# Kernel optimization log

Hardware: AMD Instinct MI355X
Metric: run time of the kernel (lower is better)

## Reference

```python
import jax, jax.numpy as jnp
import numpy as np

D_MODEL = 768
D_STATE = 16
EXPAND = 2
D_INNER = D_MODEL * EXPAND
K_CONV = 4
RMS_EPS = 1.1920928955078125e-07  # torch.finfo(float32).eps (nn.RMSNorm default eps=None)


def setup_inputs() -> dict:
    key = jax.random.key(0)
    ks = jax.random.split(key, 8)
    x = jax.random.normal(ks[0], (2, 2048, D_MODEL), dtype=jnp.float32)
    # parameters (torch Linear stores [out, in]; we keep that layout and use x @ W.T)
    in_proj_w = jax.random.normal(ks[1], (2 * D_INNER, D_MODEL), jnp.float32) * (1.0 / np.sqrt(D_MODEL))
    conv_w = jax.random.normal(ks[2], (D_INNER, 1, K_CONV), jnp.float32) * (1.0 / np.sqrt(K_CONV))
    conv_b = jax.random.normal(ks[3], (D_INNER,), jnp.float32) * 0.1
    x_proj_w = jax.random.normal(ks[4], (2 * D_STATE, D_INNER), jnp.float32) * (1.0 / np.sqrt(D_INNER))
    dt_proj_w = jax.random.normal(ks[5], (D_INNER, D_INNER), jnp.float32) * (1.0 / np.sqrt(D_INNER))
    dt_proj_b = jax.random.normal(ks[6], (D_INNER,), jnp.float32) * 0.1
    A_log = jnp.log(jnp.broadcast_to(jnp.arange(1, D_STATE + 1, dtype=jnp.float32)[None, :], (D_INNER, D_STATE)))
    D_skip = jnp.ones((D_INNER,), jnp.float32)
    out_proj_w = jax.random.normal(ks[7], (D_MODEL, D_INNER), jnp.float32) * (1.0 / np.sqrt(D_INNER))
    norm_w = jnp.ones((D_MODEL,), jnp.float32)
    return {"x": x, "norm_w": norm_w, "in_proj_w": in_proj_w, "conv_w": conv_w,
            "conv_b": conv_b, "x_proj_w": x_proj_w, "dt_proj_w": dt_proj_w,
            "dt_proj_b": dt_proj_b, "A_log": A_log, "D_skip": D_skip,
            "out_proj_w": out_proj_w}


def reference(x, norm_w, in_proj_w, conv_w, conv_b, x_proj_w, dt_proj_w,
              dt_proj_b, A_log, D_skip, out_proj_w):
    # x: [B, L, d_model]
    residual = x
    xn = x * jax.lax.rsqrt(jnp.mean(x * x, axis=-1, keepdims=True) + RMS_EPS) * norm_w
    xz = xn @ in_proj_w.T                       # [B, L, 2*d_inner]
    d_inner = in_proj_w.shape[0] // 2
    xb, z = xz[..., :d_inner], xz[..., d_inner:]
    # causal depthwise conv: torch pads 3 both sides then truncates to L == left-pad 3
    xc = jax.lax.conv_general_dilated(
        xb.transpose(0, 2, 1), conv_w, window_strides=(1,), padding=[(K_CONV - 1, 0)],
        feature_group_count=d_inner, dimension_numbers=("NCH", "OIH", "NCH"))
    xc = xc + conv_b[None, :, None]
    u = jax.nn.silu(xc.transpose(0, 2, 1))      # [B, L, d_inner]
    bc = u @ x_proj_w.T                          # [B, L, 2*d_state]
    N = A_log.shape[1]
    Bp, Cp = bc[..., :N], bc[..., N:]
    delta = jax.nn.softplus(u @ dt_proj_w.T + dt_proj_b)  # [B, L, d_inner]
    A = -jnp.exp(A_log)                          # [d_inner, N]

    def step(h, ins):
        dl, ut, Bt, Ct = ins                     # [B,D], [B,D], [B,N], [B,N]
        dA = jnp.exp(dl[:, :, None] * A)         # [B, D, N]
        h = dA * h + dl[:, :, None] * Bt[:, None, :] * ut[:, :, None]
        y = jnp.einsum("bdn,bn->bd", h, Ct)
        return h, y

    B_, L, _ = u.shape
    h0 = jnp.zeros((B_, d_inner, N), x.dtype)
    xs = (delta.transpose(1, 0, 2), u.transpose(1, 0, 2),
          Bp.transpose(1, 0, 2), Cp.transpose(1, 0, 2))
    _, ys = jax.lax.scan(step, h0, xs)           # ys: [L, B, d_inner]
    y = ys.transpose(1, 0, 2) + u * D_skip
    out = (y * jax.nn.silu(z)) @ out_proj_w.T
    return out + residual
```

## Files before the change

### kernel.cpp

```cpp
#include <hip/hip_runtime.h>
#include <math.h>

#define DM 768
#define DI 1536
#define NS 16
#define LL 2048
#define MROWS 4096
#define CH 32
#define NC 64

using bf16x8 = __attribute__((ext_vector_type(8))) short;
using f32x4 = __attribute__((ext_vector_type(4))) float;

__device__ __forceinline__ float4 ld4(const float* p) { return *(const float4*)p; }

__device__ __forceinline__ unsigned short f2bf(float f) {
  unsigned int u = __float_as_uint(f);
  u += 0x7fff + ((u >> 16) & 1);
  return (unsigned short)(u >> 16);
}
__device__ __forceinline__ float b2f(unsigned short s) {
  return __uint_as_float(((unsigned int)s) << 16);
}

__device__ __forceinline__ void gload16(const void* g, void* l) {
  __builtin_amdgcn_global_load_lds((const __attribute__((address_space(1))) void*)g,
                                   (__attribute__((address_space(3))) void*)l, 16, 0, 0);
}

#define N4_IN 589824
#define N4_CAT 638976
#define N4_OUT 294912
#define CVT_BLOCKS 5953
__global__ __launch_bounds__(256) void prep_kernel(const float* __restrict__ ipw,
                                                   const float* __restrict__ dtw,
                                                   const float* __restrict__ xpw,
                                                   const float* __restrict__ opw,
                                                   unsigned short* __restrict__ d_in4,
                                                   unsigned short* __restrict__ d_cat,
                                                   unsigned short* __restrict__ d_out4,
                                                   const float* __restrict__ x,
                                                   const float* __restrict__ nw,
                                                   unsigned short* __restrict__ xn) {
  int blk = blockIdx.x;
  int tid = threadIdx.x;
  if (blk >= CVT_BLOCKS) {
    int row = blk - CVT_BLOCKS;
    const float* xr = x + (size_t)row * DM;
    unsigned short* xo = xn + (size_t)row * DM;
    float v0 = xr[tid], v1 = xr[tid + 256], v2 = xr[tid + 512];
    float ss = v0 * v0 + v1 * v1 + v2 * v2;
#pragma unroll
    for (int o = 32; o > 0; o >>= 1) ss += __shfl_xor(ss, o, 64);
    __shared__ float red[4];
    if ((tid & 63) == 0) red[tid >> 6] = ss;
    __syncthreads();
    float tot = red[0] + red[1] + red[2] + red[3];
    float sc = rsqrtf(tot * (1.0f / 768.0f) + 1.1920928955078125e-07f);
    xo[tid] = f2bf(v0 * sc * nw[tid]);
    xo[tid + 256] = f2bf(v1 * sc * nw[tid + 256]);
    xo[tid + 512] = f2bf(v2 * sc * nw[tid + 512]);
    return;
  }
  int i = blk * 256 + tid;
  if (i < N4_IN) {
    float4 v = ld4(ipw + (size_t)i * 4);
    ushort4 o = {f2bf(v.x), f2bf(v.y), f2bf(v.z), f2bf(v.w)};
    *(ushort4*)(d_in4 + (size_t)i * 4) = o;
  } else if (i < N4_IN + N4_CAT) {
    int j = i - N4_IN;
    int row = j / 384;
    int col = (j % 384) * 4;
    ushort4 o = {0, 0, 0, 0};
    if (row < 1536) {
      float4 v = ld4(dtw + (size_t)row * DI + col);
      o = {f2bf(v.x), f2bf(v.y), f2bf(v.z), f2bf(v.w)};
    } else if (row < 1568) {
      float4 v = ld4(xpw + (size_t)(row - 1536) * DI + col);
      o = {f2bf(v.x), f2bf(v.y), f2bf(v.z), f2bf(v.w)};
    }
    *(ushort4*)(d_cat + (size_t)j * 4) = o;
  } else if (i < N4_IN + N4_CAT + N4_OUT) {
    int j = i - N4_IN - N4_CAT;
    float4 v = ld4(opw + (size_t)j * 4);
    ushort4 o = {f2bf(v.x), f2bf(v.y), f2bf(v.z), f2bf(v.w)};
    *(ushort4*)(d_out4 + (size_t)j * 4) = o;
  }
}

template <int EPI, int BM, int BN>
__global__ __launch_bounds__(256) void mfma_gemm(const unsigned short* __restrict__ A,
                                                 const unsigned short* __restrict__ Bw,
                                                 const float* __restrict__ bias,
                                                 const float* __restrict__ resid,
                                                 void* __restrict__ o0v,
                                                 void* __restrict__ o1v, int K, int gx) {
  constexpr int NFI = BM / 32;
  constexpr int NFJ = BN / 32;
  constexpr int NCH = (BM + BN) / 8;
  __shared__ unsigned short As[2][BM * 64];
  __shared__ unsigned short Bs[2][BN * 64];
  int tid = threadIdx.x;
  int lane = tid & 63, w = tid >> 6;
  int wr = w >> 1, wc = w & 1;

  int nwg = gx * gridDim.y;
  int orig = blockIdx.y * gx + blockIdx.x;
  int q = nwg >> 3;
  int swz = (orig & 7) * q + (orig >> 3);
  int bm = (swz / gx) * BM, bn = (swz % gx) * BN;

  f32x4 acc[NFI][NFJ];
#pragma unroll
  for (int i = 0; i < NFI; i++)
#pragma unroll
    for (int j = 0; j < NFJ; j++) acc[i][j] = (f32x4){0.f, 0.f, 0.f, 0.f};

  const unsigned short* Ab = A + (size_t)bm * K;
  const unsigned short* Bb = Bw + (size_t)bn * K;
  int lrow = lane >> 3;
  int kof = ((lane & 7) ^ lrow) * 8;

  auto stage = [&](int kh, int k0) {
#pragma unroll
    for (int ch = w; ch < NCH; ch += 4) {
      if (ch < BM / 8) {
        int row = ch * 8 + lrow;
        gload16(Ab + (size_t)row * K + k0 + kof, &As[kh][ch * 512]);
      } else {
        int row = (ch - BM / 8) * 8 + lrow;
        gload16(Bb + (size_t)row * K + k0 + kof, &Bs[kh][(ch - BM / 8) * 512]);
      }
    }
  };
  auto compute = [&](int kh) {
#pragma unroll
    for (int kk = 0; kk < 2; kk++) {
      int sa = (((kk * 4) + (lane >> 4)) ^ (lane & 7)) * 8;
      bf16x8 af[NFI], bfr[NFJ];
#pragma unroll
      for (int i = 0; i < NFI; i++) {
        int arow = wr * (BM / 2) + i * 16 + (lane & 15);
        af[i] = *(const bf16x8*)&As[kh][arow * 64 + sa];
      }
#pragma unroll
      for (int j = 0; j < NFJ; j++) {
        int brow = wc * (BN / 2) + j * 16 + (lane & 15);
        bfr[j] = *(const bf16x8*)&Bs[kh][brow * 64 + sa];
      }
#pragma unroll
      for (int i = 0; i < NFI; i++)
#pragma unroll
        for (int j = 0; j < NFJ; j++)
          acc[i][j] = __builtin_amdgcn_mfma_f32_16x16x32_bf16(af[i], bfr[j], acc[i][j], 0, 0, 0);
    }
  };

  int nk = K >> 7;
  for (int t = 0; t < nk; t++) {
    __syncthreads();
    stage(0, t << 7);
    stage(1, (t << 7) + 64);
    __syncthreads();
    compute(0);
    compute(1);
  }

#pragma unroll
  for (int i = 0; i < NFI; i++) {
#pragma unroll
    for (int j = 0; j < NFJ; j++) {
      int row0 = bm + wr * (BM / 2) + i * 16 + (lane >> 4) * 4;
      int col = bn + wc * (BN / 2) + j * 16 + (lane & 15);
#pragma unroll
      for (int r = 0; r < 4; r++) {
        float v = acc[i][j][r];
        int row = row0 + r;
        if (EPI == 0) {
          unsigned short* xb = (unsigned short*)o0v;
          unsigned short* z = (unsigned short*)o1v;
          if (col < DI) xb[(size_t)row * DI + col] = f2bf(v);
          else z[(size_t)row * DI + col - DI] = f2bf(v);
        } else if (EPI == 1) {
          unsigned short* delta = (unsigned short*)o0v;
          float* bc = (float*)o1v;
          if (col < DI) {
            v += bias[col];
            v = (v > 20.0f) ? v : log1pf(expf(v));
            delta[(size_t)row * DI + col] = f2bf(v);
          } else if (col < DI + 2 * NS) {
            bc[(size_t)row * 32 + col - DI] = v;
          }
        } else {
          float* out = (float*)o0v;
          out[(size_t)row * DM + col] = v + resid[(size_t)row * DM + col];
        }
      }
    }
  }
}

__global__ __launch_bounds__(192) void conv_silu_kernel(const unsigned short* __restrict__ xb,
                                                        const float* __restrict__ cw,
                                                        const float* __restrict__ cb,
                                                        unsigned short* __restrict__ u) {
  int d = (blockIdx.x * 192 + threadIdx.x) << 2;
  int m = blockIdx.y;
  int t = m & (LL - 1);
  float4 w0 = ld4(cw + d * 4);
  float4 w1 = ld4(cw + d * 4 + 4);
  float4 w2 = ld4(cw + d * 4 + 8);
  float4 w3 = ld4(cw + d * 4 + 12);
  float4 acc = {cb[d], cb[d + 1], cb[d + 2], cb[d + 3]};
#pragma unroll
  for (int tap = 0; tap < 4; tap++) {
    int dt_ = 3 - tap;
    if (t >= dt_) {
      ushort4 xv = *(const ushort4*)(xb + (size_t)(m - dt_) * DI + d);
      float wx = (tap == 0) ? w0.x : (tap == 1) ? w0.y : (tap == 2) ? w0.z : w0.w;
      float wy = (tap == 0) ? w1.x : (tap == 1) ? w1.y : (tap == 2) ? w1.z : w1.w;
      float wz = (tap == 0) ? w2.x : (tap == 1) ? w2.y : (tap == 2) ? w2.z : w2.w;
      float ww = (tap == 0) ? w3.x : (tap == 1) ? w3.y : (tap == 2) ? w3.z : w3.w;
      acc.x += b2f(xv.x) * wx;
      acc.y += b2f(xv.y) * wy;
      acc.z += b2f(xv.z) * wz;
      acc.w += b2f(xv.w) * ww;
    }
  }
  ushort4 o = {f2bf(acc.x / (1.0f + __expf(-acc.x))), f2bf(acc.y / (1.0f + __expf(-acc.y))),
               f2bf(acc.z / (1.0f + __expf(-acc.z))), f2bf(acc.w / (1.0f + __expf(-acc.w)))};
  *(ushort4*)(u + (size_t)m * DI + d) = o;
}

__global__ __launch_bounds__(256) void scan_pass1(const unsigned short* __restrict__ delta,
                                                  const unsigned short* __restrict__ u,
                                                  const float* __restrict__ bc,
                                                  const float* __restrict__ A_log,
                                                  float* __restrict__ chunkP,
                                                  float* __restrict__ chunkS) {
  int d = blockIdx.x * 256 + threadIdx.x;
  int c = blockIdx.y;
  int b = blockIdx.z;
  float Acoef[NS];
#pragma unroll
  for (int n = 0; n < NS; n++) Acoef[n] = -__expf(A_log[d * NS + n]);
  __shared__ float sB[CH][NS];
  const float* bcb = bc + (size_t)(b * LL + c * CH) * 32;
  for (int i = threadIdx.x; i < CH * NS; i += 256) sB[i >> 4][i & 15] = bcb[(i >> 4) * 32 + (i & 15)];
  __syncthreads();
  float P[NS], S[NS];
#pragma unroll
  for (int n = 0; n < NS; n++) { P[n] = 1.f; S[n] = 0.f; }
  int m0 = b * LL + c * CH;
  for (int tt = 0; tt < CH; tt++) {
    size_t off = (size_t)(m0 + tt) * DI + d;
    float dl = b2f(delta[off]);
    float ut = b2f(u[off]);
    float dlu = dl * ut;
#pragma unroll
    for (int n = 0; n < NS; n++) {
      float dA = __expf(dl * Acoef[n]);
      S[n] = dA * S[n] + dlu * sB[tt][n];
      P[n] *= dA;
    }
  }
  size_t base = ((size_t)(b * NC + c) * NS) * DI + d;
#pragma unroll
  for (int n = 0; n < NS; n++) {
    chunkP[base + (size_t)n * DI] = P[n];
    chunkS[base + (size_t)n * DI] = S[n];
  }
}

__global__ __launch_bounds__(256) void scan_pass2(const float* __restrict__ chunkP,
                                                  float* __restrict__ chunkS) {
  int id = blockIdx.x * 256 + threadIdx.x;
  int d = id % DI;
  int n = (id / DI) % NS;
  int b = id / (DI * NS);
  float h = 0.f;
  for (int c = 0; c < NC; c++) {
    size_t idx = ((size_t)(b * NC + c) * NS + n) * DI + d;
    float p = chunkP[idx];
    float s = chunkS[idx];
    chunkS[idx] = h;
    h = p * h + s;
  }
}

__global__ __launch_bounds__(256) void scan_pass3(const unsigned short* __restrict__ delta,
                                                  const unsigned short* __restrict__ u,
                                                  const float* __restrict__ bc,
                                                  const float* __restrict__ hIn,
                                                  const float* __restrict__ A_log,
                                                  const float* __restrict__ D_skip,
                                                  const unsigned short* __restrict__ z,
                                                  unsigned short* __restrict__ yg) {
  int d = blockIdx.x * 256 + threadIdx.x;
  int c = blockIdx.y;
  int b = blockIdx.z;
  float Acoef[NS];
#pragma unroll
  for (int n = 0; n < NS; n++) Acoef[n] = -__expf(A_log[d * NS + n]);
  float Dsk = D_skip[d];
  __shared__ float sBC[CH][32];
  const float* bcb = bc + (size_t)(b * LL + c * CH) * 32;
  for (int i = threadIdx.x; i < CH * 32; i += 256) sBC[i >> 5][i & 31] = bcb[i];
  __syncthreads();
  float h[NS];
  size_t base = ((size_t)(b * NC + c) * NS) * DI + d;
#pragma unroll
  for (int n = 0; n < NS; n++) h[n] = hIn[base + (size_t)n * DI];
  int m0 = b * LL + c * CH;
  for (int tt = 0; tt < CH; tt++) {
    size_t m = (size_t)(m0 + tt);
    size_t off = m * DI + d;
    float dl = b2f(delta[off]);
    float ut = b2f(u[off]);
    float dlu = dl * ut;
    float yt = 0.f;
#pragma unroll
    for (int n = 0; n < NS; n++) {
      float dA = __expf(dl * Acoef[n]);
      h[n] = dA * h[n] + dlu * sBC[tt][n];
      yt += h[n] * sBC[tt][16 + n];
    }
    float zv = b2f(z[m * DI + d]);
    float sz = zv / (1.0f + __expf(-zv));
    yg[m * DI + d] = f2bf((yt + ut * Dsk) * sz);
  }
}

extern "C" void kernel_launch(void* const* d_in, const int* in_sizes, int n_in,
                              void* d_out, int out_size, void* d_ws, size_t ws_size,
                              hipStream_t stream) {
  const float* x = (const float*)d_in[0];
  const float* norm_w = (const float*)d_in[1];
  const float* in_proj_w = (const float*)d_in[2];
  const float* conv_w = (const float*)d_in[3];
  const float* conv_b = (const float*)d_in[4];
  const float* x_proj_w = (const float*)d_in[5];
  const float* dt_proj_w = (const float*)d_in[6];
  const float* dt_proj_b = (const float*)d_in[7];
  const float* A_log = (const float*)d_in[8];
  const float* D_skip = (const float*)d_in[9];
  const float* out_proj_w = (const float*)d_in[10];
  float* out = (float*)d_out;

  float* ws = (float*)d_ws;
  unsigned short* xb_bf = (unsigned short*)ws;
  unsigned short* z_bf = (unsigned short*)(ws + 3145728);
  unsigned short* u_bf = (unsigned short*)(ws + 6291456);
  unsigned short* delta_bf = (unsigned short*)(ws + 9437184);
  unsigned short* ygbf = (unsigned short*)(ws + 15728640);
  unsigned short* wbf_in = (unsigned short*)(ws + 18874368);
  unsigned short* wbf_cat = (unsigned short*)(ws + 20054016);
  unsigned short* wbf_out = (unsigned short*)(ws + 21331968);
  float* chunkP = ws + 21921792;
  float* chunkS = ws + 25067520;
  unsigned short* xn_bf = (unsigned short*)d_out;
  float* bcb = (float*)d_out + 1572864;

  prep_kernel<<<CVT_BLOCKS + 4096, 256, 0, stream>>>(in_proj_w, dt_proj_w, x_proj_w,
                                                     out_proj_w, wbf_in, wbf_cat, wbf_out,
                                                     x, norm_w, xn_bf);

  mfma_gemm<0, 64, 64><<<dim3(48, 64), 256, 0, stream>>>(xn_bf, wbf_in, nullptr, nullptr,
                                                         xb_bf, z_bf, DM, 48);

  conv_silu_kernel<<<dim3(2, 4096), 192, 0, stream>>>(xb_bf, conv_w, conv_b, u_bf);

  mfma_gemm<1, 64, 64><<<dim3(26, 64), 256, 0, stream>>>(u_bf, wbf_cat, dt_proj_b, nullptr,
                                                         delta_bf, bcb, DI, 26);

  scan_pass1<<<dim3(6, NC, 2), 256, 0, stream>>>(delta_bf, u_bf, bcb, A_log, chunkP, chunkS);
  scan_pass2<<<192, 256, 0, stream>>>(chunkP, chunkS);
  scan_pass3<<<dim3(6, NC, 2), 256, 0, stream>>>(delta_bf, u_bf, bcb, chunkS, A_log, D_skip,
                                                 z_bf, ygbf);

  mfma_gemm<2, 64, 64><<<dim3(12, 64), 256, 0, stream>>>(ygbf, wbf_out, nullptr, x, out,
                                                         nullptr, DI, 12);
}
```

Baseline: 218.0 us.

## Add dedicated producer wave to GEMM for double-buffered load/compute overlap

Adds a fifth wavefront to the bf16 MFMA GEMM that acts only as a producer. It streams the next 64-wide K slice into the alternate LDS buffer while the four compute waves run MFMAs on the current one. The per-iteration K step drops from 128 to 64, and the separate stage/sync/compute phases become a single barrier per step. This aims to hide global-load latency behind matrix math, at the cost of a serial single-wave loader, more barriers, and an extra wave per block.

```diff
diff --git a/kernel.cpp b/kernel.cpp
--- a/kernel.cpp
+++ b/kernel.cpp
@@ -89,7 +89,7 @@
 }
 
 template <int EPI, int BM, int BN>
-__global__ __launch_bounds__(256) void mfma_gemm(const unsigned short* __restrict__ A,
+__global__ __launch_bounds__(320) void mfma_gemm(const unsigned short* __restrict__ A,
                                                  const unsigned short* __restrict__ Bw,
                                                  const float* __restrict__ bias,
                                                  const float* __restrict__ resid,
@@ -102,7 +102,7 @@
   __shared__ unsigned short Bs[2][BN * 64];
   int tid = threadIdx.x;
   int lane = tid & 63, w = tid >> 6;
-  int wr = w >> 1, wc = w & 1;
+  int wr = (w & 3) >> 1, wc = w & 1;
 
   int nwg = gx * gridDim.y;
   int orig = blockIdx.y * gx + blockIdx.x;
@@ -121,19 +121,19 @@
   int lrow = lane >> 3;
   int kof = ((lane & 7) ^ lrow) * 8;
 
-  auto stage = [&](int kh, int k0) {
-#pragma unroll
-    for (int ch = w; ch < NCH; ch += 4) {
+  auto stagep = [&](int buf, int k0) {
+#pragma unroll
+    for (int ch = 0; ch < NCH; ch++) {
       if (ch < BM / 8) {
         int row = ch * 8 + lrow;
-        gload16(Ab + (size_t)row * K + k0 + kof, &As[kh][ch * 512]);
+        gload16(Ab + (size_t)row * K + k0 + kof, &As[buf][ch * 512]);
       } else {
         int row = (ch - BM / 8) * 8 + lrow;
-        gload16(Bb + (size_t)row * K + k0 + kof, &Bs[kh][(ch - BM / 8) * 512]);
+        gload16(Bb + (size_t)row * K + k0 + kof, &Bs[buf][(ch - BM / 8) * 512]);
       }
     }
   };
-  auto compute = [&](int kh) {
+  auto compute = [&](int buf) {
 #pragma unroll
     for (int kk = 0; kk < 2; kk++) {
       int sa = (((kk * 4) + (lane >> 4)) ^ (lane & 7)) * 8;
@@ -141,12 +141,12 @@
 #pragma unroll
       for (int i = 0; i < NFI; i++) {
         int arow = wr * (BM / 2) + i * 16 + (lane & 15);
-        af[i] = *(const bf16x8*)&As[kh][arow * 64 + sa];
+        af[i] = *(const bf16x8*)&As[buf][arow * 64 + sa];
       }
 #pragma unroll
       for (int j = 0; j < NFJ; j++) {
         int brow = wc * (BN / 2) + j * 16 + (lane & 15);
-        bfr[j] = *(const bf16x8*)&Bs[kh][brow * 64 + sa];
+        bfr[j] = *(const bf16x8*)&Bs[buf][brow * 64 + sa];
       }
 #pragma unroll
       for (int i = 0; i < NFI; i++)
@@ -156,44 +156,54 @@
     }
   };
 
-  int nk = K >> 7;
+  int nk = K >> 6;
+  if (w == 4) {
+    stagep(0, 0);
+    asm volatile("s_waitcnt vmcnt(0)" ::: "memory");
+  }
+  __syncthreads();
   for (int t = 0; t < nk; t++) {
+    if (w == 4) {
+      if (t + 1 < nk) {
+        stagep((t + 1) & 1, (t + 1) << 6);
+        asm volatile("s_waitcnt vmcnt(0)" ::: "memory");
+      }
+    } else {
+      compute(t & 1);
+    }
     __syncthreads();
-    stage(0, t << 7);
-    stage(1, (t << 7) + 64);
-    __syncthreads();
-    compute(0);
-    compute(1);
-  }
-
-#pragma unroll
-  for (int i = 0; i < NFI; i++) {
-#pragma unroll
-    for (int j = 0; j < NFJ; j++) {
-      int row0 = bm + wr * (BM / 2) + i * 16 + (lane >> 4) * 4;
-      int col = bn + wc * (BN / 2) + j * 16 + (lane & 15);
-#pragma unroll
-      for (int r = 0; r < 4; r++) {
-        float v = acc[i][j][r];
-        int row = row0 + r;
-        if (EPI == 0) {
-          unsigned short* xb = (unsigned short*)o0v;
-          unsigned short* z = (unsigned short*)o1v;
-          if (col < DI) xb[(size_t)row * DI + col] = f2bf(v);
-          else z[(size_t)row * DI + col - DI] = f2bf(v);
-        } else if (EPI == 1) {
-          unsigned short* delta = (unsigned short*)o0v;
-          float* bc = (float*)o1v;
-          if (col < DI) {
-            v += bias[col];
-            v = (v > 20.0f) ? v : log1pf(expf(v));
-            delta[(size_t)row * DI + col] = f2bf(v);
-          } else if (col < DI + 2 * NS) {
-            bc[(size_t)row * 32 + col - DI] = v;
+  }
+
+  if (w < 4) {
+#pragma unroll
+    for (int i = 0; i < NFI; i++) {
+#pragma unroll
+      for (int j = 0; j < NFJ; j++) {
+        int row0 = bm + wr * (BM / 2) + i * 16 + (lane >> 4) * 4;
+        int col = bn + wc * (BN / 2) + j * 16 + (lane & 15);
+#pragma unroll
+        for (int r = 0; r < 4; r++) {
+          float v = acc[i][j][r];
+          int row = row0 + r;
+          if (EPI == 0) {
+            unsigned short* xb = (unsigned short*)o0v;
+            unsigned short* z = (unsigned short*)o1v;
+            if (col < DI) xb[(size_t)row * DI + col] = f2bf(v);
+            else z[(size_t)row * DI + col - DI] = f2bf(v);
+          } else if (EPI == 1) {
+            unsigned short* delta = (unsigned short*)o0v;
+            float* bc = (float*)o1v;
+            if (col < DI) {
+              v += bias[col];
+              v = (v > 20.0f) ? v : log1pf(expf(v));
+              delta[(size_t)row * DI + col] = f2bf(v);
+            } else if (col < DI + 2 * NS) {
+              bc[(size_t)row * 32 + col - DI] = v;
+            }
+          } else {
+            float* out = (float*)o0v;
+            out[(size_t)row * DM + col] = v + resid[(size_t)row * DM + col];
           }
-        } else {
-          float* out = (float*)o0v;
-          out[(size_t)row * DM + col] = v + resid[(size_t)row * DM + col];
         }
       }
     }
@@ -365,12 +375,12 @@
                                                      out_proj_w, wbf_in, wbf_cat, wbf_out,
                                                      x, norm_w, xn_bf);
 
-  mfma_gemm<0, 64, 64><<<dim3(48, 64), 256, 0, stream>>>(xn_bf, wbf_in, nullptr, nullptr,
+  mfma_gemm<0, 64, 64><<<dim3(48, 64), 320, 0, stream>>>(xn_bf, wbf_in, nullptr, nullptr,
                                                          xb_bf, z_bf, DM, 48);
 
   conv_silu_kernel<<<dim3(2, 4096), 192, 0, stream>>>(xb_bf, conv_w, conv_b, u_bf);
 
-  mfma_gemm<1, 64, 64><<<dim3(26, 64), 256, 0, stream>>>(u_bf, wbf_cat, dt_proj_b, nullptr,
+  mfma_gemm<1, 64, 64><<<dim3(26, 64), 320, 0, stream>>>(u_bf, wbf_cat, dt_proj_b, nullptr,
                                                          delta_bf, bcb, DI, 26);
 
   scan_pass1<<<dim3(6, NC, 2), 256, 0, stream>>>(delta_bf, u_bf, bcb, A_log, chunkP, chunkS);
@@ -378,6 +388,6 @@
   scan_pass3<<<dim3(6, NC, 2), 256, 0, stream>>>(delta_bf, u_bf, bcb, chunkS, A_log, D_skip,
                                                  z_bf, ygbf);
 
-  mfma_gemm<2, 64, 64><<<dim3(12, 64), 256, 0, stream>>>(ygbf, wbf_out, nullptr, x, out,
+  mfma_gemm<2, 64, 64><<<dim3(12, 64), 320, 0, stream>>>(ygbf, wbf_out, nullptr, x, out,
                                                          nullptr, DI, 12);
 }
```

New measurement: 242.5 us. 11.2% more time.
